# Kernel optimization log

Hardware: AMD Instinct MI355X
Metric: run time of the kernel (lower is better)

Reference implementation:

```python
import jax, jax.numpy as jnp
import numpy as np

INPUT_SIZE = 64
HIDDEN = 128
BATCH = 512
SEQ = 512


def setup_inputs() -> dict:
    key = jax.random.key(0)
    ks = jax.random.split(key, 7)
    s_ih = 1.0 / np.sqrt(HIDDEN)
    token = jax.random.normal(ks[0], (BATCH, SEQ, INPUT_SIZE), dtype=jnp.float32)
    W_ih = jax.random.uniform(ks[1], (HIDDEN, INPUT_SIZE), jnp.float32, -s_ih, s_ih)
    W_hh = jax.random.uniform(ks[2], (HIDDEN, HIDDEN), jnp.float32, -s_ih, s_ih)
    b_ih = jax.random.uniform(ks[3], (HIDDEN,), jnp.float32, -s_ih, s_ih)
    b_hh = jax.random.uniform(ks[4], (HIDDEN,), jnp.float32, -s_ih, s_ih)
    W_lin = jax.random.uniform(ks[5], (1, HIDDEN), jnp.float32, -s_ih, s_ih)
    b_lin = jax.random.uniform(ks[6], (1,), jnp.float32, -s_ih, s_ih)
    return {"token": token, "W_ih": W_ih, "W_hh": W_hh, "b_ih": b_ih,
            "b_hh": b_hh, "W_lin": W_lin, "b_lin": b_lin}


def reference(token, W_ih, W_hh, b_ih, b_hh, W_lin, b_lin):
    # Precompute input projection for all timesteps: [T, B, H]
    x_proj = jnp.einsum('bti,hi->tbh', token, W_ih) + b_ih + b_hh
    h0 = jnp.zeros((token.shape[0], W_hh.shape[0]), dtype=token.dtype)

    def step(h, xp):
        h_new = jnp.tanh(xp + h @ W_hh.T)
        return h_new, None

    h_last, _ = jax.lax.scan(step, h0, x_proj)
    # Linear head on last hidden state: [B, 1]
    return h_last @ W_lin.T + b_lin
```

## Files before the change

### kernel.cpp

```cpp
#include <hip/hip_runtime.h>

#define B_ 512
#define T_ 512
#define I_ 64
#define H_ 128

#define HB0    0
#define HB1    256
#define DUMMY  512
#define LDS_SZ 1536

#define FM(a, x, w) "v_fmac_f32 v" #a ", v" #x ", v" #w "\n\t"
#define SC(n) "v_mul_f32 v" #n ", 0x4038aa3b, v" #n "\n\t"

#define CLOBS \
    "v48","v49","v50","v51","v52","v53","v54","v55","v56","v57","v58","v59", \
    "v60","v61","v62","v63","v64","v65","v66","v67","v68","v69","v70","v71", \
    "v72","v73","v74","v75","v76","v77","v78","v79","v80","v81","v82","v83", \
    "v84","v85","v86","v87","v88","v89","v90","v91","v92","v93","v94","v95", \
    "v96","v97","v98","v99","v100","v101","v102","v103","v104","v105","v106", \
    "v107","v108","v109","v110","v111","v112","v113","v114","v115","v116", \
    "v117","v118","v119","v120","v121","v122","v123","v124","v125","v126", \
    "v127","memory"

#define RNN_STEP(TA, TB, TC, TD, HRD, HWR)                                    \
    asm volatile(                                                             \
        "ds_read_b128 v[72:75], %1\n\t"                                       \
        "s_waitcnt vmcnt(3)\n\t"                                              \
        "v_fma_f32 v48, v" #TA ", v112, %3\n\t"                               \
        "v_fma_f32 v49, v" #TA ", v116, %4\n\t"                               \
        "v_fma_f32 v50, v" #TA ", v120, %5\n\t"                               \
        "v_fma_f32 v51, v" #TA ", v124, %6\n\t"                               \
        FM(48,TB,113) FM(49,TB,117) FM(50,TB,121) FM(51,TB,125)               \
        FM(48,TC,114) FM(49,TC,118) FM(50,TC,122) FM(51,TC,126)               \
        FM(48,TD,115) FM(49,TD,119) FM(50,TD,123) FM(51,TD,127)               \
        "global_load_dwordx4 v[" #TA ":" #TD "], %0, %9\n\t"                  \
        "v_add_u32 %0, 0x100, %0\n\t"                                         \
        "v_and_b32 %0, 0x1ffff, %0\n\t"                                       \
        "s_waitcnt lgkmcnt(0)\n\t"                                            \
        "v_dot2_f32_bf16 v48, v72, v80, v48\n\t"                              \
        "v_dot2_f32_bf16 v49, v72, v84, v49\n\t"                              \
        "v_dot2_f32_bf16 v50, v72, v88, v50\n\t"                              \
        "v_dot2_f32_bf16 v51, v72, v92, v51\n\t"                              \
        "v_dot2_f32_bf16 v48, v73, v81, v48\n\t"                              \
        "v_dot2_f32_bf16 v49, v73, v85, v49\n\t"                              \
        "v_dot2_f32_bf16 v50, v73, v89, v50\n\t"                              \
        "v_dot2_f32_bf16 v51, v73, v93, v51\n\t"                              \
        "v_dot2_f32_bf16 v48, v74, v82, v48\n\t"                              \
        "v_dot2_f32_bf16 v49, v74, v86, v49\n\t"                              \
        "v_dot2_f32_bf16 v50, v74, v90, v50\n\t"                              \
        "v_dot2_f32_bf16 v51, v74, v94, v51\n\t"                              \
        "v_dot2_f32_bf16 v48, v75, v83, v48\n\t"                              \
        "v_dot2_f32_bf16 v49, v75, v87, v49\n\t"                              \
        "v_dot2_f32_bf16 v50, v75, v91, v50\n\t"                              \
        "v_dot2_f32_bf16 v51, v75, v95, v51\n\t"                              \
        "s_nop 1\n\t"                                                         \
        "v_add_f32 v48, v48, v48 quad_perm:[1,0,3,2] row_mask:0xf bank_mask:0xf\n\t" \
        "v_add_f32 v49, v49, v49 quad_perm:[1,0,3,2] row_mask:0xf bank_mask:0xf\n\t" \
        "v_add_f32 v50, v50, v50 quad_perm:[1,0,3,2] row_mask:0xf bank_mask:0xf\n\t" \
        "v_add_f32 v51, v51, v51 quad_perm:[1,0,3,2] row_mask:0xf bank_mask:0xf\n\t" \
        "v_cndmask_b32 v52, v48, v49, %7\n\t"                                 \
        "v_cndmask_b32 v53, v50, v51, %7\n\t"                                 \
        "s_nop 0\n\t"                                                         \
        "v_add_f32 v52, v52, v52 quad_perm:[2,3,0,1] row_mask:0xf bank_mask:0xf\n\t" \
        "v_add_f32 v53, v53, v53 quad_perm:[2,3,0,1] row_mask:0xf bank_mask:0xf\n\t" \
        "v_cndmask_b32 v54, v52, v53, %8\n\t"                                 \
        "s_nop 1\n\t"                                                         \
        "v_add_f32 v54, v54, v54 row_shl:8 row_mask:0xf bank_mask:0x3\n\t"    \
        "s_nop 1\n\t"                                                         \
        "v_add_f32 v54, v54, v54 row_shl:4 row_mask:0xf bank_mask:0x1\n\t"    \
        "s_nop 1\n\t"                                                         \
        "v_exp_f32 v54, v54\n\t"                                              \
        "s_nop 0\n\t"                                                         \
        "v_add_f32 v54, 1.0, v54\n\t"                                         \
        "v_rcp_f32 v55, v54\n\t"                                              \
        "s_nop 0\n\t"                                                         \
        "v_fma_f32 v54, v55, -2.0, 1.0\n\t"                                   \
        "v_cvt_pk_bf16_f32 v54, v54, v54\n\t"                                 \
        "ds_write_b16 %2, v54\n\t"                                            \
        "s_waitcnt lgkmcnt(0)\n\t"                                            \
        "s_barrier"                                                           \
        : "+v"(voff)                                                          \
        : "v"(HRD), "v"(HWR), "v"(biasA), "v"(biasB), "v"(biasC),             \
          "v"(biasD), "s"(M1), "s"(M2), "s"(sbase)                            \
        : CLOBS)

__global__ __launch_bounds__(512) __attribute__((amdgpu_waves_per_eu(4, 4)))
void rnn_kernel(const float* __restrict__ token,
                const float* __restrict__ W_ih,
                const float* __restrict__ W_hh,
                const float* __restrict__ b_ih,
                const float* __restrict__ b_hh,
                const float* __restrict__ W_lin,
                const float* __restrict__ b_lin,
                float* __restrict__ out)
{
    __shared__ __align__(16) char lds[LDS_SZ];
    const unsigned lb =
        (unsigned)(uintptr_t)(__attribute__((address_space(3))) char*)lds;

    const int tid = threadIdx.x;
    const int e   = tid & 15;
    const int G   = tid >> 4;
    const int b   = blockIdx.x;
    const int jb  = 4 * G;

    {
        const float* pWh = W_hh + jb * H_ + e * 8;
        asm volatile(
            "global_load_dwordx4 v[48:51], %0, off\n\t"
            "global_load_dwordx4 v[52:55], %0, off offset:16\n\t"
            "global_load_dwordx4 v[56:59], %0, off offset:512\n\t"
            "global_load_dwordx4 v[60:63], %0, off offset:528\n\t"
            "global_load_dwordx4 v[64:67], %0, off offset:1024\n\t"
            "global_load_dwordx4 v[68:71], %0, off offset:1040\n\t"
            "global_load_dwordx4 v[72:75], %0, off offset:1536\n\t"
            "global_load_dwordx4 v[76:79], %0, off offset:1552\n\t"
            "s_waitcnt vmcnt(0)\n\t"
            SC(48) SC(49) SC(50) SC(51) SC(52) SC(53) SC(54) SC(55)
            SC(56) SC(57) SC(58) SC(59) SC(60) SC(61) SC(62) SC(63)
            SC(64) SC(65) SC(66) SC(67) SC(68) SC(69) SC(70) SC(71)
            SC(72) SC(73) SC(74) SC(75) SC(76) SC(77) SC(78) SC(79)
            "v_cvt_pk_bf16_f32 v80, v48, v49\n\t"
            "v_cvt_pk_bf16_f32 v81, v50, v51\n\t"
            "v_cvt_pk_bf16_f32 v82, v52, v53\n\t"
            "v_cvt_pk_bf16_f32 v83, v54, v55\n\t"
            "v_cvt_pk_bf16_f32 v84, v56, v57\n\t"
            "v_cvt_pk_bf16_f32 v85, v58, v59\n\t"
            "v_cvt_pk_bf16_f32 v86, v60, v61\n\t"
            "v_cvt_pk_bf16_f32 v87, v62, v63\n\t"
            "v_cvt_pk_bf16_f32 v88, v64, v65\n\t"
            "v_cvt_pk_bf16_f32 v89, v66, v67\n\t"
            "v_cvt_pk_bf16_f32 v90, v68, v69\n\t"
            "v_cvt_pk_bf16_f32 v91, v70, v71\n\t"
            "v_cvt_pk_bf16_f32 v92, v72, v73\n\t"
            "v_cvt_pk_bf16_f32 v93, v74, v75\n\t"
            "v_cvt_pk_bf16_f32 v94, v76, v77\n\t"
            "v_cvt_pk_bf16_f32 v95, v78, v79\n\t"
            :: "v"(pWh) : CLOBS);
    }
    {
        const float* pWi = W_ih + jb * I_ + e * 4;
        asm volatile(
            "global_load_dwordx4 v[112:115], %0, off\n\t"
            "global_load_dwordx4 v[116:119], %0, off offset:256\n\t"
            "global_load_dwordx4 v[120:123], %0, off offset:512\n\t"
            "global_load_dwordx4 v[124:127], %0, off offset:768\n\t"
            "s_waitcnt vmcnt(0)\n\t"
            SC(112) SC(113) SC(114) SC(115) SC(116) SC(117) SC(118) SC(119)
            SC(120) SC(121) SC(122) SC(123) SC(124) SC(125) SC(126) SC(127)
            :: "v"(pWi) : CLOBS);
    }

    const float k16 = 2.885390081777927f / 16.0f;
    const float biasA = (b_ih[jb + 0] + b_hh[jb + 0]) * k16;
    const float biasB = (b_ih[jb + 1] + b_hh[jb + 1]) * k16;
    const float biasC = (b_ih[jb + 2] + b_hh[jb + 2]) * k16;
    const float biasD = (b_ih[jb + 3] + b_hh[jb + 3]) * k16;
    const unsigned long long M1 = 0xAAAAAAAAAAAAAAAAULL;
    const unsigned long long M2 = 0xCCCCCCCCCCCCCCCCULL;

    const int  jsel   = jb + (e & 3);
    const bool writer = (e < 4);
    const unsigned dmy = lb + DUMMY + tid * 2;
    const unsigned hw0 = writer ? (lb + HB1 + jsel * 2) : dmy;
    const unsigned hw1 = writer ? (lb + HB0 + jsel * 2) : dmy;
    const unsigned hr0 = lb + HB0 + e * 16;
    const unsigned hr1 = lb + HB1 + e * 16;

    const float* tok_row = token + (size_t)b * T_ * I_;
    const unsigned long long sbase = (unsigned long long)(uintptr_t)tok_row;

    {
        const unsigned v0 = e * 16;
        asm volatile(
            "global_load_dwordx4 v[56:59], %0, %1\n\t"
            "global_load_dwordx4 v[60:63], %0, %1 offset:256\n\t"
            "global_load_dwordx4 v[64:67], %0, %1 offset:512\n\t"
            "global_load_dwordx4 v[68:71], %0, %1 offset:768\n\t"
            :: "v"(v0), "s"(sbase) : CLOBS);
    }
    unsigned voff = e * 16 + 1024;
    if (tid < H_) *(unsigned short*)(lds + HB0 + tid * 2) = 0;
    asm volatile("s_waitcnt lgkmcnt(0)\n\ts_barrier" ::: "memory");

#pragma unroll 1
    for (int t = 0; t < T_; t += 4) {
        RNN_STEP(56, 57, 58, 59, hr0, hw0);
        RNN_STEP(60, 61, 62, 63, hr1, hw1);
        RNN_STEP(64, 65, 66, 67, hr0, hw0);
        RNN_STEP(68, 69, 70, 71, hr1, hw1);
    }

    asm volatile("s_waitcnt vmcnt(0)" ::: "memory");

    if (tid < 64) {
        unsigned u0 = *(const unsigned short*)(lds + HB0 + 2 * tid);
        unsigned u1 = *(const unsigned short*)(lds + HB0 + 2 * (tid + 64));
        float h0 = __uint_as_float(u0 << 16);
        float h1 = __uint_as_float(u1 << 16);
        float p = h0 * W_lin[tid] + h1 * W_lin[tid + 64];
#pragma unroll
        for (int off = 32; off; off >>= 1) p += __shfl_down(p, off);
        if (tid == 0) out[b] = p + b_lin[0];
    }
}

extern "C" void kernel_launch(void* const* d_in, const int* in_sizes, int n_in,
                              void* d_out, int out_size, void* d_ws, size_t ws_size,
                              hipStream_t stream) {
    const float* token = (const float*)d_in[0];
    const float* W_ih  = (const float*)d_in[1];
    const float* W_hh  = (const float*)d_in[2];
    const float* b_ih  = (const float*)d_in[3];
    const float* b_hh  = (const float*)d_in[4];
    const float* W_lin = (const float*)d_in[5];
    const float* b_lin = (const float*)d_in[6];
    float* out = (float*)d_out;

    hipLaunchKernelGGL(rnn_kernel, dim3(B_), dim3(512), 0, stream,
                       token, W_ih, W_hh, b_ih, b_hh, W_lin, b_lin, out);
}
```

Before: 208.4 us.

## Compute eight hidden units per lane group and halve block size

Each 16-lane group now produces eight hidden outputs per step instead of four, so W_hh and W_ih are held for twice as many rows in registers. The block shrinks from 512 to 256 threads with two waves per EU. The goal is to halve redundant token loads and per-output reduction work, make the per-step barrier cheaper with fewer waves, and overlap two exp/rcp chains for more ILP. In exchange, each wave does twice the arithmetic per timestep on a serial critical path, and there are fewer waves to hide latency.

```diff
diff --git a/kernel.cpp b/kernel.cpp
--- a/kernel.cpp
+++ b/kernel.cpp
@@ -8,84 +8,108 @@
 #define HB0    0
 #define HB1    256
 #define DUMMY  512
-#define LDS_SZ 1536
-
-#define FM(a, x, w) "v_fmac_f32 v" #a ", v" #x ", v" #w "\n\t"
-#define SC(n) "v_mul_f32 v" #n ", 0x4038aa3b, v" #n "\n\t"
+#define LDS_SZ 768
+
+#define FM(a,x,w)  "v_fmac_f32 v" #a ", v" #x ", v" #w "\n\t"
+#define DT(A,X,W)  "v_dot2_f32_bf16 v" #A ", v" #X ", v" #W ", v" #A "\n\t"
+#define PK(D,LO,HI) "v_cvt_pk_bf16_f32 v" #D ", v" #LO ", v" #HI "\n\t"
+#define SC(n)      "v_mul_f32 v" #n ", 0x4038aa3b, v" #n "\n\t"
+#define LDW(A,B,OFF) "global_load_dwordx4 v[" #A ":" #B "], %0, off offset:" #OFF "\n\t"
 
 #define CLOBS \
-    "v48","v49","v50","v51","v52","v53","v54","v55","v56","v57","v58","v59", \
-    "v60","v61","v62","v63","v64","v65","v66","v67","v68","v69","v70","v71", \
-    "v72","v73","v74","v75","v76","v77","v78","v79","v80","v81","v82","v83", \
-    "v84","v85","v86","v87","v88","v89","v90","v91","v92","v93","v94","v95", \
-    "v96","v97","v98","v99","v100","v101","v102","v103","v104","v105","v106", \
-    "v107","v108","v109","v110","v111","v112","v113","v114","v115","v116", \
-    "v117","v118","v119","v120","v121","v122","v123","v124","v125","v126", \
-    "v127","memory"
-
-#define RNN_STEP(TA, TB, TC, TD, HRD, HWR)                                    \
+    "v20","v21","v22","v23","v24","v25","v26","v27","v28","v29","v30","v31", \
+    "v32","v33","v34","v35","v36","v37","v38","v39","v40","v41","v42","v43", \
+    "v44","v45","v46","v47","v48","v49","v50","v51","v52","v53","v54","v55", \
+    "v56","v57","v58","v59","v60","v61","v62","v63","v64","v65","v66","v67", \
+    "v68","v69","v70","v71","v72","v73","v74","v75","v76","v77","v78","v79", \
+    "v80","v81","v82","v83","v84","v85","v86","v87","v88","v89","v90","v91", \
+    "v92","v93","v94","v95","v96","v97","v98","v99","v100","v101","v102", \
+    "v103","v104","v105","v106","v107","v108","v109","v110","v111","v112", \
+    "v113","v114","v115","v116","v117","v118","v119","memory"
+
+#define RNN_STEP(TA, TB, TC, TD, HRD, HWA, HWB)                               \
     asm volatile(                                                             \
-        "ds_read_b128 v[72:75], %1\n\t"                                       \
+        "ds_read_b128 v[36:39], %1\n\t"                                       \
         "s_waitcnt vmcnt(3)\n\t"                                              \
-        "v_fma_f32 v48, v" #TA ", v112, %3\n\t"                               \
-        "v_fma_f32 v49, v" #TA ", v116, %4\n\t"                               \
-        "v_fma_f32 v50, v" #TA ", v120, %5\n\t"                               \
-        "v_fma_f32 v51, v" #TA ", v124, %6\n\t"                               \
-        FM(48,TB,113) FM(49,TB,117) FM(50,TB,121) FM(51,TB,125)               \
-        FM(48,TC,114) FM(49,TC,118) FM(50,TC,122) FM(51,TC,126)               \
-        FM(48,TD,115) FM(49,TD,119) FM(50,TD,123) FM(51,TD,127)               \
-        "global_load_dwordx4 v[" #TA ":" #TD "], %0, %9\n\t"                  \
+        "v_fma_f32 v20, v" #TA ", v56, %4\n\t"                                \
+        "v_fma_f32 v21, v" #TA ", v60, %5\n\t"                                \
+        "v_fma_f32 v22, v" #TA ", v64, %6\n\t"                                \
+        "v_fma_f32 v23, v" #TA ", v68, %7\n\t"                                \
+        "v_fma_f32 v24, v" #TA ", v72, %8\n\t"                                \
+        "v_fma_f32 v25, v" #TA ", v76, %9\n\t"                                \
+        "v_fma_f32 v26, v" #TA ", v80, %10\n\t"                               \
+        "v_fma_f32 v27, v" #TA ", v84, %11\n\t"                               \
+        FM(20,TB,57) FM(21,TB,61) FM(22,TB,65) FM(23,TB,69)                   \
+        FM(24,TB,73) FM(25,TB,77) FM(26,TB,81) FM(27,TB,85)                   \
+        FM(20,TC,58) FM(21,TC,62) FM(22,TC,66) FM(23,TC,70)                   \
+        FM(24,TC,74) FM(25,TC,78) FM(26,TC,82) FM(27,TC,86)                   \
+        FM(20,TD,59) FM(21,TD,63) FM(22,TD,67) FM(23,TD,71)                   \
+        FM(24,TD,75) FM(25,TD,79) FM(26,TD,83) FM(27,TD,87)                   \
+        "global_load_dwordx4 v[" #TA ":" #TD "], %0, %14\n\t"                 \
         "v_add_u32 %0, 0x100, %0\n\t"                                         \
         "v_and_b32 %0, 0x1ffff, %0\n\t"                                       \
         "s_waitcnt lgkmcnt(0)\n\t"                                            \
-        "v_dot2_f32_bf16 v48, v72, v80, v48\n\t"                              \
-        "v_dot2_f32_bf16 v49, v72, v84, v49\n\t"                              \
-        "v_dot2_f32_bf16 v50, v72, v88, v50\n\t"                              \
-        "v_dot2_f32_bf16 v51, v72, v92, v51\n\t"                              \
-        "v_dot2_f32_bf16 v48, v73, v81, v48\n\t"                              \
-        "v_dot2_f32_bf16 v49, v73, v85, v49\n\t"                              \
-        "v_dot2_f32_bf16 v50, v73, v89, v50\n\t"                              \
-        "v_dot2_f32_bf16 v51, v73, v93, v51\n\t"                              \
-        "v_dot2_f32_bf16 v48, v74, v82, v48\n\t"                              \
-        "v_dot2_f32_bf16 v49, v74, v86, v49\n\t"                              \
-        "v_dot2_f32_bf16 v50, v74, v90, v50\n\t"                              \
-        "v_dot2_f32_bf16 v51, v74, v94, v51\n\t"                              \
-        "v_dot2_f32_bf16 v48, v75, v83, v48\n\t"                              \
-        "v_dot2_f32_bf16 v49, v75, v87, v49\n\t"                              \
-        "v_dot2_f32_bf16 v50, v75, v91, v50\n\t"                              \
-        "v_dot2_f32_bf16 v51, v75, v95, v51\n\t"                              \
+        DT(20,36,88)  DT(21,36,92)  DT(22,36,96)  DT(23,36,100)               \
+        DT(24,36,104) DT(25,36,108) DT(26,36,112) DT(27,36,116)               \
+        DT(20,37,89)  DT(21,37,93)  DT(22,37,97)  DT(23,37,101)               \
+        DT(24,37,105) DT(25,37,109) DT(26,37,113) DT(27,37,117)               \
+        DT(20,38,90)  DT(21,38,94)  DT(22,38,98)  DT(23,38,102)               \
+        DT(24,38,106) DT(25,38,110) DT(26,38,114) DT(27,38,118)               \
+        DT(20,39,91)  DT(21,39,95)  DT(22,39,99)  DT(23,39,103)               \
+        DT(24,39,107) DT(25,39,111) DT(26,39,115) DT(27,39,119)               \
+                  \
+        "v_add_f32 v20, v20, v20 quad_perm:[1,0,3,2] row_mask:0xf bank_mask:0xf\n\t" \
+        "v_add_f32 v21, v21, v21 quad_perm:[1,0,3,2] row_mask:0xf bank_mask:0xf\n\t" \
+        "v_add_f32 v22, v22, v22 quad_perm:[1,0,3,2] row_mask:0xf bank_mask:0xf\n\t" \
+        "v_add_f32 v23, v23, v23 quad_perm:[1,0,3,2] row_mask:0xf bank_mask:0xf\n\t" \
+        "v_add_f32 v24, v24, v24 quad_perm:[1,0,3,2] row_mask:0xf bank_mask:0xf\n\t" \
+        "v_add_f32 v25, v25, v25 quad_perm:[1,0,3,2] row_mask:0xf bank_mask:0xf\n\t" \
+        "v_add_f32 v26, v26, v26 quad_perm:[1,0,3,2] row_mask:0xf bank_mask:0xf\n\t" \
+        "v_add_f32 v27, v27, v27 quad_perm:[1,0,3,2] row_mask:0xf bank_mask:0xf\n\t" \
+        "v_cndmask_b32 v28, v20, v21, %12\n\t"                                \
+        "v_cndmask_b32 v29, v22, v23, %12\n\t"                                \
+        "v_cndmask_b32 v30, v24, v25, %12\n\t"                                \
+        "v_cndmask_b32 v31, v26, v27, %12\n\t"                                \
+                                         \
+        "v_add_f32 v28, v28, v28 quad_perm:[2,3,0,1] row_mask:0xf bank_mask:0xf\n\t" \
+        "v_add_f32 v29, v29, v29 quad_perm:[2,3,0,1] row_mask:0xf bank_mask:0xf\n\t" \
+        "v_add_f32 v30, v30, v30 quad_perm:[2,3,0,1] row_mask:0xf bank_mask:0xf\n\t" \
+        "v_add_f32 v31, v31, v31 quad_perm:[2,3,0,1] row_mask:0xf bank_mask:0xf\n\t" \
+        "v_cndmask_b32 v32, v28, v29, %13\n\t"                                \
+        "v_cndmask_b32 v33, v30, v31, %13\n\t"                                \
+        "s_nop 0\n\t"                                                         \
+                   \
+        "v_add_f32 v32, v32, v32 row_shl:8 row_mask:0xf bank_mask:0x3\n\t"    \
+        "v_add_f32 v33, v33, v33 row_shl:8 row_mask:0xf bank_mask:0x3\n\t"    \
+        "s_nop 0\n\t"                                                         \
+             \
+        "v_add_f32 v32, v32, v32 row_shl:4 row_mask:0xf bank_mask:0x1\n\t"    \
+        "v_add_f32 v33, v33, v33 row_shl:4 row_mask:0xf bank_mask:0x1\n\t"    \
         "s_nop 1\n\t"                                                         \
-        "v_add_f32 v48, v48, v48 quad_perm:[1,0,3,2] row_mask:0xf bank_mask:0xf\n\t" \
-        "v_add_f32 v49, v49, v49 quad_perm:[1,0,3,2] row_mask:0xf bank_mask:0xf\n\t" \
-        "v_add_f32 v50, v50, v50 quad_perm:[1,0,3,2] row_mask:0xf bank_mask:0xf\n\t" \
-        "v_add_f32 v51, v51, v51 quad_perm:[1,0,3,2] row_mask:0xf bank_mask:0xf\n\t" \
-        "v_cndmask_b32 v52, v48, v49, %7\n\t"                                 \
-        "v_cndmask_b32 v53, v50, v51, %7\n\t"                                 \
-        "s_nop 0\n\t"                                                         \
-        "v_add_f32 v52, v52, v52 quad_perm:[2,3,0,1] row_mask:0xf bank_mask:0xf\n\t" \
-        "v_add_f32 v53, v53, v53 quad_perm:[2,3,0,1] row_mask:0xf bank_mask:0xf\n\t" \
-        "v_cndmask_b32 v54, v52, v53, %8\n\t"                                 \
-        "s_nop 1\n\t"                                                         \
-        "v_add_f32 v54, v54, v54 row_shl:8 row_mask:0xf bank_mask:0x3\n\t"    \
-        "s_nop 1\n\t"                                                         \
-        "v_add_f32 v54, v54, v54 row_shl:4 row_mask:0xf bank_mask:0x1\n\t"    \
-        "s_nop 1\n\t"                                                         \
-        "v_exp_f32 v54, v54\n\t"                                              \
-        "s_nop 0\n\t"                                                         \
-        "v_add_f32 v54, 1.0, v54\n\t"                                         \
-        "v_rcp_f32 v55, v54\n\t"                                              \
-        "s_nop 0\n\t"                                                         \
-        "v_fma_f32 v54, v55, -2.0, 1.0\n\t"                                   \
-        "v_cvt_pk_bf16_f32 v54, v54, v54\n\t"                                 \
-        "ds_write_b16 %2, v54\n\t"                                            \
+        "v_exp_f32 v34, v32\n\t"                                              \
+        "v_exp_f32 v35, v33\n\t"                                              \
+        "s_nop 0\n\t"                                                         \
+        "v_add_f32 v34, 1.0, v34\n\t"                                         \
+        "v_add_f32 v35, 1.0, v35\n\t"                                         \
+        "v_rcp_f32 v34, v34\n\t"                                              \
+        "v_rcp_f32 v35, v35\n\t"                                              \
+        "s_nop 0\n\t"                                                         \
+        "v_fma_f32 v34, v34, -2.0, 1.0\n\t"                                   \
+        "v_fma_f32 v35, v35, -2.0, 1.0\n\t"                                   \
+        "v_cvt_pk_bf16_f32 v34, v34, v34\n\t"                                 \
+        "v_cvt_pk_bf16_f32 v35, v35, v35\n\t"                                 \
+        "ds_write_b16 %2, v34\n\t"                                            \
+        "ds_write_b16 %3, v35\n\t"                                            \
         "s_waitcnt lgkmcnt(0)\n\t"                                            \
         "s_barrier"                                                           \
         : "+v"(voff)                                                          \
-        : "v"(HRD), "v"(HWR), "v"(biasA), "v"(biasB), "v"(biasC),             \
-          "v"(biasD), "s"(M1), "s"(M2), "s"(sbase)                            \
+        : "v"(HRD), "v"(HWA), "v"(HWB),                                       \
+          "v"(bias0), "v"(bias1), "v"(bias2), "v"(bias3),                     \
+          "v"(bias4), "v"(bias5), "v"(bias6), "v"(bias7),                     \
+          "s"(M1), "s"(M2), "s"(sbase)                                        \
         : CLOBS)
 
-__global__ __launch_bounds__(512) __attribute__((amdgpu_waves_per_eu(4, 4)))
+__global__ __launch_bounds__(256) __attribute__((amdgpu_waves_per_eu(2, 2)))
 void rnn_kernel(const float* __restrict__ token,
                 const float* __restrict__ W_ih,
                 const float* __restrict__ W_hh,
@@ -103,81 +127,79 @@
     const int e   = tid & 15;
     const int G   = tid >> 4;
     const int b   = blockIdx.x;
-    const int jb  = 4 * G;
+    const int jb  = 8 * G;
 
     {
         const float* pWh = W_hh + jb * H_ + e * 8;
         asm volatile(
-            "global_load_dwordx4 v[48:51], %0, off\n\t"
-            "global_load_dwordx4 v[52:55], %0, off offset:16\n\t"
-            "global_load_dwordx4 v[56:59], %0, off offset:512\n\t"
-            "global_load_dwordx4 v[60:63], %0, off offset:528\n\t"
-            "global_load_dwordx4 v[64:67], %0, off offset:1024\n\t"
-            "global_load_dwordx4 v[68:71], %0, off offset:1040\n\t"
-            "global_load_dwordx4 v[72:75], %0, off offset:1536\n\t"
-            "global_load_dwordx4 v[76:79], %0, off offset:1552\n\t"
+            LDW(56,59,0)    LDW(60,63,16)   LDW(64,67,512)  LDW(68,71,528)
+            LDW(72,75,1024) LDW(76,79,1040) LDW(80,83,1536) LDW(84,87,1552)
             "s_waitcnt vmcnt(0)\n\t"
-            SC(48) SC(49) SC(50) SC(51) SC(52) SC(53) SC(54) SC(55)
             SC(56) SC(57) SC(58) SC(59) SC(60) SC(61) SC(62) SC(63)
             SC(64) SC(65) SC(66) SC(67) SC(68) SC(69) SC(70) SC(71)
             SC(72) SC(73) SC(74) SC(75) SC(76) SC(77) SC(78) SC(79)
-            "v_cvt_pk_bf16_f32 v80, v48, v49\n\t"
-            "v_cvt_pk_bf16_f32 v81, v50, v51\n\t"
-            "v_cvt_pk_bf16_f32 v82, v52, v53\n\t"
-            "v_cvt_pk_bf16_f32 v83, v54, v55\n\t"
-            "v_cvt_pk_bf16_f32 v84, v56, v57\n\t"
-            "v_cvt_pk_bf16_f32 v85, v58, v59\n\t"
-            "v_cvt_pk_bf16_f32 v86, v60, v61\n\t"
-            "v_cvt_pk_bf16_f32 v87, v62, v63\n\t"
-            "v_cvt_pk_bf16_f32 v88, v64, v65\n\t"
-            "v_cvt_pk_bf16_f32 v89, v66, v67\n\t"
-            "v_cvt_pk_bf16_f32 v90, v68, v69\n\t"
-            "v_cvt_pk_bf16_f32 v91, v70, v71\n\t"
-            "v_cvt_pk_bf16_f32 v92, v72, v73\n\t"
-            "v_cvt_pk_bf16_f32 v93, v74, v75\n\t"
-            "v_cvt_pk_bf16_f32 v94, v76, v77\n\t"
-            "v_cvt_pk_bf16_f32 v95, v78, v79\n\t"
+            SC(80) SC(81) SC(82) SC(83) SC(84) SC(85) SC(86) SC(87)
+            PK(88,56,57)  PK(89,58,59)  PK(90,60,61)  PK(91,62,63)
+            PK(92,64,65)  PK(93,66,67)  PK(94,68,69)  PK(95,70,71)
+            PK(96,72,73)  PK(97,74,75)  PK(98,76,77)  PK(99,78,79)
+            PK(100,80,81) PK(101,82,83) PK(102,84,85) PK(103,86,87)
+            LDW(56,59,2048) LDW(60,63,2064) LDW(64,67,2560) LDW(68,71,2576)
+            LDW(72,75,3072) LDW(76,79,3088) LDW(80,83,3584) LDW(84,87,3600)
+            "s_waitcnt vmcnt(0)\n\t"
+            SC(56) SC(57) SC(58) SC(59) SC(60) SC(61) SC(62) SC(63)
+            SC(64) SC(65) SC(66) SC(67) SC(68) SC(69) SC(70) SC(71)
+            SC(72) SC(73) SC(74) SC(75) SC(76) SC(77) SC(78) SC(79)
+            SC(80) SC(81) SC(82) SC(83) SC(84) SC(85) SC(86) SC(87)
+            PK(104,56,57) PK(105,58,59) PK(106,60,61) PK(107,62,63)
+            PK(108,64,65) PK(109,66,67) PK(110,68,69) PK(111,70,71)
+            PK(112,72,73) PK(113,74,75) PK(114,76,77) PK(115,78,79)
+            PK(116,80,81) PK(117,82,83) PK(118,84,85) PK(119,86,87)
             :: "v"(pWh) : CLOBS);
     }
     {
         const float* pWi = W_ih + jb * I_ + e * 4;
         asm volatile(
-            "global_load_dwordx4 v[112:115], %0, off\n\t"
-            "global_load_dwordx4 v[116:119], %0, off offset:256\n\t"
-            "global_load_dwordx4 v[120:123], %0, off offset:512\n\t"
-            "global_load_dwordx4 v[124:127], %0, off offset:768\n\t"
+            LDW(56,59,0)    LDW(60,63,256)  LDW(64,67,512)  LDW(68,71,768)
+            LDW(72,75,1024) LDW(76,79,1280) LDW(80,83,1536) LDW(84,87,1792)
             "s_waitcnt vmcnt(0)\n\t"
-            SC(112) SC(113) SC(114) SC(115) SC(116) SC(117) SC(118) SC(119)
-            SC(120) SC(121) SC(122) SC(123) SC(124) SC(125) SC(126) SC(127)
+            SC(56) SC(57) SC(58) SC(59) SC(60) SC(61) SC(62) SC(63)
+            SC(64) SC(65) SC(66) SC(67) SC(68) SC(69) SC(70) SC(71)
+            SC(72) SC(73) SC(74) SC(75) SC(76) SC(77) SC(78) SC(79)
+            SC(80) SC(81) SC(82) SC(83) SC(84) SC(85) SC(86) SC(87)
             :: "v"(pWi) : CLOBS);
     }
 
     const float k16 = 2.885390081777927f / 16.0f;
-    const float biasA = (b_ih[jb + 0] + b_hh[jb + 0]) * k16;
-    const float biasB = (b_ih[jb + 1] + b_hh[jb + 1]) * k16;
-    const float biasC = (b_ih[jb + 2] + b_hh[jb + 2]) * k16;
-    const float biasD = (b_ih[jb + 3] + b_hh[jb + 3]) * k16;
+    const float bias0 = (b_ih[jb+0] + b_hh[jb+0]) * k16;
+    const float bias1 = (b_ih[jb+1] + b_hh[jb+1]) * k16;
+    const float bias2 = (b_ih[jb+2] + b_hh[jb+2]) * k16;
+    const float bias3 = (b_ih[jb+3] + b_hh[jb+3]) * k16;
+    const float bias4 = (b_ih[jb+4] + b_hh[jb+4]) * k16;
+    const float bias5 = (b_ih[jb+5] + b_hh[jb+5]) * k16;
+    const float bias6 = (b_ih[jb+6] + b_hh[jb+6]) * k16;
+    const float bias7 = (b_ih[jb+7] + b_hh[jb+7]) * k16;
     const unsigned long long M1 = 0xAAAAAAAAAAAAAAAAULL;
     const unsigned long long M2 = 0xCCCCCCCCCCCCCCCCULL;
 
-    const int  jsel   = jb + (e & 3);
     const bool writer = (e < 4);
-    const unsigned dmy = lb + DUMMY + tid * 2;
-    const unsigned hw0 = writer ? (lb + HB1 + jsel * 2) : dmy;
-    const unsigned hw1 = writer ? (lb + HB0 + jsel * 2) : dmy;
-    const unsigned hr0 = lb + HB0 + e * 16;
-    const unsigned hr1 = lb + HB1 + e * 16;
-
-    const float* tok_row = token + (size_t)b * T_ * I_;
-    const unsigned long long sbase = (unsigned long long)(uintptr_t)tok_row;
+    const unsigned dmy = lb + DUMMY + (tid & 63) * 4;
+    const unsigned hr0  = lb + HB0 + e * 16;
+    const unsigned hr1  = lb + HB1 + e * 16;
+    const unsigned hwa0 = writer ? (lb + HB1 + 2 * (jb + e))     : dmy;
+    const unsigned hwb0 = writer ? (lb + HB1 + 2 * (jb + 4 + e)) : dmy;
+    const unsigned hwa1 = writer ? (lb + HB0 + 2 * (jb + e))     : dmy;
+    const unsigned hwb1 = writer ? (lb + HB0 + 2 * (jb + 4 + e)) : dmy;
+
+    const unsigned long long sbase =
+        (unsigned long long)(uintptr_t)(token + (size_t)b * T_ * I_);
 
     {
         const unsigned v0 = e * 16;
         asm volatile(
-            "global_load_dwordx4 v[56:59], %0, %1\n\t"
-            "global_load_dwordx4 v[60:63], %0, %1 offset:256\n\t"
-            "global_load_dwordx4 v[64:67], %0, %1 offset:512\n\t"
-            "global_load_dwordx4 v[68:71], %0, %1 offset:768\n\t"
+            "global_load_dwordx4 v[40:43], %0, %1\n\t"
+            "global_load_dwordx4 v[44:47], %0, %1 offset:256\n\t"
+            "global_load_dwordx4 v[48:51], %0, %1 offset:512\n\t"
+            "global_load_dwordx4 v[52:55], %0, %1 offset:768\n\t"
             :: "v"(v0), "s"(sbase) : CLOBS);
     }
     unsigned voff = e * 16 + 1024;
@@ -186,10 +208,10 @@
 
 #pragma unroll 1
     for (int t = 0; t < T_; t += 4) {
-        RNN_STEP(56, 57, 58, 59, hr0, hw0);
-        RNN_STEP(60, 61, 62, 63, hr1, hw1);
-        RNN_STEP(64, 65, 66, 67, hr0, hw0);
-        RNN_STEP(68, 69, 70, 71, hr1, hw1);
+        RNN_STEP(40, 41, 42, 43, hr0, hwa0, hwb0);
+        RNN_STEP(44, 45, 46, 47, hr1, hwa1, hwb1);
+        RNN_STEP(48, 49, 50, 51, hr0, hwa0, hwb0);
+        RNN_STEP(52, 53, 54, 55, hr1, hwa1, hwb1);
     }
 
     asm volatile("s_waitcnt vmcnt(0)" ::: "memory");
@@ -218,6 +240,6 @@
     const float* b_lin = (const float*)d_in[6];
     float* out = (float*)d_out;
 
-    hipLaunchKernelGGL(rnn_kernel, dim3(B_), dim3(512), 0, stream,
+    hipLaunchKernelGGL(rnn_kernel, dim3(B_), dim3(256), 0, stream,
                        token, W_ih, W_hh, b_ih, b_hh, W_lin, b_lin, out);
 }
```

After: 225.5 us. 1.08x slower.
